# Performance work log

Hardware: AMD Instinct MI355X
Metric: run time of the kernel (lower is better)

The kernel has to match this reference:

```python
import jax, jax.numpy as jnp
import numpy as np

N_NODES = 100000
N_EDGES = 1600000
N_FEAT = 165
HIDDEN = 128
N_CLASSES = 2
NEG_SLOPE = 0.2


def setup_inputs() -> dict:
    key = jax.random.key(0)
    ks = jax.random.split(key, 16)
    s = 0.05
    return {
        'x': jax.random.normal(ks[0], (N_NODES, N_FEAT), jnp.float32),
        'edge_src': jax.random.randint(ks[1], (N_EDGES,), 0, N_NODES, jnp.int32),
        'edge_dst': jax.random.randint(ks[2], (N_EDGES,), 0, N_NODES, jnp.int32),
        'W1l': jax.random.normal(ks[3], (N_FEAT, HIDDEN), jnp.float32) * s,
        'b1l': jnp.zeros((HIDDEN,), jnp.float32),
        'W1r': jax.random.normal(ks[4], (N_FEAT, HIDDEN), jnp.float32) * s,
        'b1r': jnp.zeros((HIDDEN,), jnp.float32),
        'att1': jax.random.normal(ks[5], (HIDDEN,), jnp.float32) * s,
        'bias1': jnp.zeros((HIDDEN,), jnp.float32),
        'W2l': jax.random.normal(ks[6], (HIDDEN, N_CLASSES), jnp.float32) * s,
        'b2l': jnp.zeros((N_CLASSES,), jnp.float32),
        'W2r': jax.random.normal(ks[7], (HIDDEN, N_CLASSES), jnp.float32) * s,
        'b2r': jnp.zeros((N_CLASSES,), jnp.float32),
        'att2': jax.random.normal(ks[8], (N_CLASSES,), jnp.float32) * s,
        'bias2': jnp.zeros((N_CLASSES,), jnp.float32),
    }


def gatv2_conv(x, src, dst, Wl, bl, Wr, br, att, bias, n_nodes):
    # PyG GATv2Conv, heads=1: x_l for source/message, x_r for target
    xl = x @ Wl + bl            # [N, D_out]
    xr = x @ Wr + br            # [N, D_out]
    e = jax.nn.leaky_relu(xl[src] + xr[dst], NEG_SLOPE)  # [E, D_out]
    score = e @ att             # [E]
    # segment softmax over destination nodes (stable)
    m = jax.ops.segment_max(score, dst, num_segments=n_nodes)
    a = jnp.exp(score - m[dst])
    denom = jax.ops.segment_sum(a, dst, num_segments=n_nodes)
    alpha = a / denom[dst]      # [E]
    out = jax.ops.segment_sum(alpha[:, None] * xl[src], dst, num_segments=n_nodes)
    return out + bias


def reference(x, edge_src, edge_dst, W1l, b1l, W1r, b1r, att1, bias1,
              W2l, b2l, W2r, b2r, att2, bias2):
    n = x.shape[0]
    # GATv2Conv adds self loops by default; every node has >=1 incoming edge
    loops = jnp.arange(n, dtype=edge_src.dtype)
    src = jnp.concatenate([edge_src, loops])
    dst = jnp.concatenate([edge_dst, loops])
    h = gatv2_conv(x, src, dst, W1l, b1l, W1r, b1r, att1, bias1, n)
    h = jax.nn.relu(h)
    # F.dropout with training=False is identity (eval mode)
    out = gatv2_conv(h, src, dst, W2l, b2l, W2r, b2r, att2, bias2, n)
    return out
```

## Files before the change

### kernel.cpp

```cpp
#include <hip/hip_runtime.h>
#include <hip/hip_bf16.h>

#define N_NODES 100000
#define NPAD 100032
#define N_EDGES 1600000
#define ETOT (N_EDGES + N_NODES)
#define NFEAT 165
#define KP 192
#define HID 128
#define NCLS 2
#define NEG 0.2f

#define NBUCK 391
#define CHUNK 4096
#define NCHUNK 416
#define TOT4 ((NBUCK * NCHUNK) / 4)
#define NSB ((TOT4 + 511) / 512)
#define GS_BLOCKS 2048
#define REPACK_BLKS (NPAD / 64)

typedef short bf16x8 __attribute__((ext_vector_type(8)));
typedef float f32x4 __attribute__((ext_vector_type(4)));

#define OFF_FLAG 0
#define OFF_W 16
#define WO_ATT1 42496
#define WO_BIAS1 42624
#define WO_W2L 42752
#define WO_B2L 43008
#define WO_W2R 43010
#define WO_B2R 43266
#define WO_ATT2 43268
#define WO_BIAS2 43270

#define OFF_XB   43392
#define OFF_XP   OFF_XB
#define OFF_WT   (OFF_XB + NPAD * KP / 2)
#define OFF_BCAT (OFF_WT + 256 * KP / 2)
#define OFF_XLB  (OFF_BCAT + 256)
#define OFF_XRB  (OFF_XLB + NPAD * HID / 2)
#define OFF_PAIRS (OFF_XRB + NPAD * HID / 2)
#define OFF_CSR  (OFF_PAIRS + 2 * ETOT)
#define OFF_ROWPTR (OFF_CSR + ETOT)
#define OFF_S    (OFF_ROWPTR + N_NODES + 8)
#define OFF_XL2  (OFF_S + NBUCK * NCHUNK + 8)
#define OFF_XR2  (OFF_XL2 + N_NODES * NCLS)
#define OFF_H    (OFF_XR2 + N_NODES * NCLS)
#define OFF_DL   (OFF_H + N_NODES * HID)
#define OFF_DR   (OFF_DL + NPAD)
#define OFF_W2A  (OFF_DR + NPAD)
#define OFF_BSUM (OFF_W2A + 512)

__device__ __forceinline__ float bload16(unsigned short u) {
    return __uint_as_float(((unsigned)u) << 16);
}

__device__ __forceinline__ float lrelu(float v) {
    return fmaf(0.4f, fabsf(v), 0.6f * v);
}

__device__ __forceinline__ void unpack8(uint4 q, float* f) {
    f[0] = __uint_as_float(q.x << 16); f[1] = __uint_as_float(q.x & 0xffff0000u);
    f[2] = __uint_as_float(q.y << 16); f[3] = __uint_as_float(q.y & 0xffff0000u);
    f[4] = __uint_as_float(q.z << 16); f[5] = __uint_as_float(q.z & 0xffff0000u);
    f[6] = __uint_as_float(q.w << 16); f[7] = __uint_as_float(q.w & 0xffff0000u);
}

__device__ __forceinline__ unsigned short f2b(float f) {
    __hip_bfloat16 b = __float2bfloat16(f);
    return *(unsigned short*)&b;
}

__device__ __forceinline__ unsigned pack2(float a, float b) {
    return (unsigned)f2b(a) | ((unsigned)f2b(b) << 16);
}

__device__ __forceinline__ unsigned detect_flag(const unsigned short* x16, int lane) {
    unsigned short hh = x16[lane];
    unsigned e = (hh >> 7) & 0xFF;
    bool pl = ((hh & 0x7FFF) == 0) || (e >= 100 && e <= 140);
    unsigned long long m = __ballot(pl);
    return (__popcll(m) >= 52) ? 1u : 0u;
}

#define PREP_WT 49152
#define PREP_BC (PREP_WT + 256)
#define PREP_TOT (PREP_BC + 776)
#define PREP_BLKS ((PREP_TOT + 255) / 256)
__global__ void __launch_bounds__(256) k_prep_hist(
        const int* __restrict__ edst, int* __restrict__ bh,
        const unsigned short* __restrict__ x16,
        const void* W1l, const void* b1l, const void* W1r, const void* b1r,
        const void* att1, const void* bias1, const void* W2l, const void* b2l,
        const void* W2r, const void* b2r, const void* att2, const void* bias2,
        unsigned* __restrict__ flagp, unsigned short* __restrict__ wt,
        float* __restrict__ bcat, float* __restrict__ wb,
        float* __restrict__ w2a, unsigned short* __restrict__ xp) {
    __shared__ int hist[NBUCK];
    if (blockIdx.x < NCHUNK) {
        for (int i = threadIdx.x; i < NBUCK; i += 256) hist[i] = 0;
        __syncthreads();
        int base = blockIdx.x * CHUNK;
        for (int i = threadIdx.x; i < CHUNK; i += 256) {
            int e = base + i;
            if (e >= ETOT) break;
            int d = (e < N_EDGES) ? edst[e] : (e - N_EDGES);
            atomicAdd(&hist[d >> 8], 1);
        }
        __syncthreads();
        for (int b = threadIdx.x; b < NBUCK; b += 256)
            bh[b * NCHUNK + blockIdx.x] = hist[b];
        return;
    }
    int lane = threadIdx.x & 63;
    unsigned isbf = detect_flag(x16, lane);
    const float* xf = (const float*)x16;

    if (blockIdx.x >= NCHUNK + PREP_BLKS) {
        int node0 = (blockIdx.x - NCHUNK - PREP_BLKS) * 64;
        for (int i = threadIdx.x; i < 64 * (KP / 8); i += 256) {
            int r = i / (KP / 8);
            int c0 = (i - r * (KP / 8)) * 8;
            int grow = node0 + r;
            unsigned short hh[8];
#pragma unroll
            for (int j = 0; j < 8; j++) {
                int c = c0 + j;
                unsigned short v = 0;
                if (grow < N_NODES && c < NFEAT) {
                    size_t g = (size_t)grow * NFEAT + c;
                    v = isbf ? x16[g] : f2b(xf[g]);
                }
                hh[j] = v;
            }
            uint4 o;
            o.x = (unsigned)hh[0] | ((unsigned)hh[1] << 16);
            o.y = (unsigned)hh[2] | ((unsigned)hh[3] << 16);
            o.z = (unsigned)hh[4] | ((unsigned)hh[5] << 16);
            o.w = (unsigned)hh[6] | ((unsigned)hh[7] << 16);
            *(uint4*)&xp[(size_t)grow * KP + c0] = o;
        }
        return;
    }

    int i = (blockIdx.x - NCHUNK) * 256 + threadIdx.x;
    if (i == 0) *flagp = isbf;
    if (i >= PREP_TOT) return;
    if (i < PREP_WT) {
        int n = i / KP, k = i - n * KP;
        unsigned short v = 0;
        if (k < NFEAT) {
            const void* src = (n < HID) ? W1l : W1r;
            size_t off = (size_t)k * HID + (n & (HID - 1));
            v = isbf ? ((const unsigned short*)src)[off]
                     : f2b(((const float*)src)[off]);
        }
        wt[i] = v;
    } else if (i < PREP_BC) {
        int n = i - PREP_WT;
        const void* src = (n < HID) ? b1l : b1r;
        int off = n & (HID - 1);
        bcat[n] = isbf ? bload16(((const unsigned short*)src)[off])
                       : ((const float*)src)[off];
    } else {
        int j = i - PREP_BC;
        const void* src; int off; int dst;
        if      (j < 128) { src = att1;  off = j;       dst = WO_ATT1 + j; }
        else if (j < 256) { src = bias1; off = j - 128; dst = WO_BIAS1 + (j - 128); }
        else if (j < 512) { src = W2l;   off = j - 256; dst = WO_W2L + (j - 256); }
        else if (j < 514) { src = b2l;   off = j - 512; dst = WO_B2L + (j - 512); }
        else if (j < 770) { src = W2r;   off = j - 514; dst = WO_W2R + (j - 514); }
        else if (j < 772) { src = b2r;   off = j - 770; dst = WO_B2R + (j - 770); }
        else if (j < 774) { src = att2;  off = j - 772; dst = WO_ATT2 + (j - 772); }
        else              { src = bias2; off = j - 774; dst = WO_BIAS2 + (j - 774); }
        float val = isbf ? bload16(((const unsigned short*)src)[off])
                         : ((const float*)src)[off];
        wb[dst] = val;
        if (j >= 256 && j < 512) w2a[j - 256] = val;
        else if (j >= 514 && j < 770) w2a[256 + (j - 514)] = val;
    }
}

__global__ void __launch_bounds__(512) k_scan1(const int* __restrict__ S,
                                               int* __restrict__ bsum) {
    __shared__ int lds[512];
    int t = threadIdx.x;
    int i = blockIdx.x * 512 + t;
    const uint4* S4 = (const uint4*)S;
    int v = 0;
    if (i < TOT4) {
        uint4 q = S4[i];
        v = (int)(q.x + q.y + q.z + q.w);
    }
    lds[t] = v;
    __syncthreads();
    for (int off = 256; off > 0; off >>= 1) {
        if (t < off) lds[t] += lds[t + off];
        __syncthreads();
    }
    if (t == 0) bsum[blockIdx.x] = lds[0];
}

__global__ void __launch_bounds__(128) k_scan2(int* __restrict__ bsum) {
    __shared__ int lds[128];
    int t = threadIdx.x;
    int v = (t < NSB) ? bsum[t] : 0;
    lds[t] = v;
    __syncthreads();
    for (int off = 1; off < 128; off <<= 1) {
        int x = lds[t];
        if (t >= off) x += lds[t - off];
        __syncthreads();
        lds[t] = x;
        __syncthreads();
    }
    if (t < NSB) bsum[t] = (t == 0) ? 0 : lds[t - 1];
}

__global__ void __launch_bounds__(512) k_scan3(int* __restrict__ S,
                                               const int* __restrict__ bsum,
                                               int* __restrict__ rowptr) {
    __shared__ int lds[512];
    int t = threadIdx.x, b = blockIdx.x;
    int i = b * 512 + t;
    uint4* S4 = (uint4*)S;
    uint4 q = {0, 0, 0, 0};
    if (i < TOT4) q = S4[i];
    int s = (int)(q.x + q.y + q.z + q.w);
    lds[t] = s;
    __syncthreads();
    for (int off = 1; off < 512; off <<= 1) {
        int x = lds[t];
        if (t >= off) x += lds[t - off];
        __syncthreads();
        lds[t] = x;
        __syncthreads();
    }
    int excl = ((t == 0) ? 0 : lds[t - 1]) + bsum[b];
    if (i < TOT4) {
        uint4 o;
        o.x = excl;
        o.y = excl + q.x;
        o.z = excl + q.x + q.y;
        o.w = excl + q.x + q.y + q.z;
        S4[i] = o;
    }
    if (b == 0 && t == 0) rowptr[N_NODES] = ETOT;
}

__global__ void __launch_bounds__(256) k_scatter(const int* __restrict__ esrc,
                                                 const int* __restrict__ edst,
                                                 const int* __restrict__ S,
                                                 unsigned* __restrict__ pairs) {
    __shared__ int cur[NBUCK];
    for (int i = threadIdx.x; i < NBUCK; i += 256)
        cur[i] = S[i * NCHUNK + blockIdx.x];
    __syncthreads();
    int base = blockIdx.x * CHUNK;
    for (int i = threadIdx.x; i < CHUNK; i += 256) {
        int e = base + i;
        if (e >= ETOT) break;
        int s = (e < N_EDGES) ? esrc[e] : (e - N_EDGES);
        int d = (e < N_EDGES) ? edst[e] : (e - N_EDGES);
        int p = atomicAdd(&cur[d >> 8], 1);
        pairs[p] = (unsigned)s | ((unsigned)(d & 255) << 24);
    }
}

__global__ void __launch_bounds__(256) k_gemm1(
        const unsigned short* __restrict__ xp,
        const unsigned short* __restrict__ wt, const float* __restrict__ bcat,
        const float* __restrict__ attp,
        __hip_bfloat16* __restrict__ xlb, __hip_bfloat16* __restrict__ xrb,
        float* __restrict__ dl, float* __restrict__ dr) {
    __shared__ float dpart[4][64];
    int tid = threadIdx.x;
    int wave = tid >> 6, lane = tid & 63;
    int quad = lane >> 4, li = lane & 15;
    int node0 = blockIdx.x * 64;

    bf16x8 wfrag[4][6];
#pragma unroll
    for (int q = 0; q < 4; q++) {
        int n = wave * 64 + q * 16 + li;
#pragma unroll
        for (int kk = 0; kk < 6; kk++)
            wfrag[q][kk] = *(const bf16x8*)&wt[(size_t)n * KP + kk * 32 + quad * 8];
    }
    float4 bv[4], attq4[4];
    int colbase = (wave & 1) * 64;
#pragma unroll
    for (int q = 0; q < 4; q++) {
        bv[q] = *(const float4*)&bcat[wave * 64 + q * 16 + quad * 4];
        attq4[q] = *(const float4*)&attp[colbase + q * 16 + quad * 4];
    }

    for (int mt = 0; mt < 4; mt++) {
        int node = node0 + mt * 16 + li;
        bf16x8 xfrag[6];
#pragma unroll
        for (int kk = 0; kk < 6; kk++)
            xfrag[kk] = *(const bf16x8*)&xp[(size_t)node * KP + kk * 32 + quad * 8];
        __hip_bfloat16* dst = (wave < 2) ? xlb : xrb;
        float dp = 0.f;
#pragma unroll
        for (int q = 0; q < 4; q++) {
            f32x4 a = {0.f, 0.f, 0.f, 0.f};
#pragma unroll
            for (int kk = 0; kk < 6; kk++)
                a = __builtin_amdgcn_mfma_f32_16x16x32_bf16(wfrag[q][kk], xfrag[kk], a, 0, 0, 0);
            float f0 = a[0] + bv[q].x, f1 = a[1] + bv[q].y;
            float f2 = a[2] + bv[q].z, f3 = a[3] + bv[q].w;
            dp = fmaf(f0, attq4[q].x, dp);
            dp = fmaf(f1, attq4[q].y, dp);
            dp = fmaf(f2, attq4[q].z, dp);
            dp = fmaf(f3, attq4[q].w, dp);
            uint2 val = { pack2(f0, f1), pack2(f2, f3) };
            int col = colbase + q * 16 + quad * 4;
            *(uint2*)&dst[(size_t)node * HID + col] = val;
        }
        dp += __shfl_xor(dp, 16);
        dp += __shfl_xor(dp, 32);
        if (lane < 16) dpart[wave][mt * 16 + li] = dp;
    }
    __syncthreads();
    if (tid < 64)
        dl[node0 + tid] = dpart[0][tid] + dpart[1][tid];
    else if (tid < 128)
        dr[node0 + tid - 64] = dpart[2][tid - 64] + dpart[3][tid - 64];
}

__global__ void __launch_bounds__(256) k_bsort(const int* __restrict__ S,
                                               const unsigned* __restrict__ pairs,
                                               int* __restrict__ rowptr,
                                               int* __restrict__ csr) {
    __shared__ int hist[256];
    __shared__ int cur[256];
    int b = blockIdx.x, t = threadIdx.x;
    int beg = S[b * NCHUNK];
    int end = (b == NBUCK - 1) ? ETOT : S[(b + 1) * NCHUNK];
    hist[t] = 0;
    __syncthreads();
    for (int j = beg + t; j < end; j += 256)
        atomicAdd(&hist[pairs[j] >> 24], 1);
    __syncthreads();
    for (int off = 1; off < 256; off <<= 1) {
        int v = hist[t];
        if (t >= off) v += hist[t - off];
        __syncthreads();
        hist[t] = v;
        __syncthreads();
    }
    int excl = (t == 0) ? 0 : hist[t - 1];
    int node = b * 256 + t;
    if (node < N_NODES) rowptr[node] = beg + excl;
    cur[t] = beg + excl;
    __syncthreads();
    for (int j = beg + t; j < end; j += 256) {
        unsigned pr = pairs[j];
        int p = atomicAdd(&cur[pr >> 24], 1);
        csr[p] = (int)(pr & 0xFFFFFFu);
    }
}

__global__ void __launch_bounds__(256) k_gat1(const int* __restrict__ rowptr,
                                              const int* __restrict__ csr,
                                              const __hip_bfloat16* __restrict__ xlb,
                                              const __hip_bfloat16* __restrict__ xrb,
                                              const float* __restrict__ att,
                                              const float* __restrict__ bias,
                                              const float* __restrict__ dotsl,
                                              const float* __restrict__ dotsr,
                                              unsigned short* __restrict__ h16) {
    int wave = threadIdx.x >> 6, lane = threadIdx.x & 63;
    int sub = lane >> 4, li = lane & 15;
    float atv[8];
    {
        float4 t0 = ((const float4*)att)[li * 2];
        float4 t1 = ((const float4*)att)[li * 2 + 1];
        atv[0] = 0.4f * t0.x; atv[1] = 0.4f * t0.y;
        atv[2] = 0.4f * t0.z; atv[3] = 0.4f * t0.w;
        atv[4] = 0.4f * t1.x; atv[5] = 0.4f * t1.y;
        atv[6] = 0.4f * t1.z; atv[7] = 0.4f * t1.w;
    }

    for (int d = blockIdx.x * 4 + wave; d < N_NODES; d += GS_BLOCKS * 4) {
        uint4 qr = ((const uint4*)(xrb + (size_t)d * HID))[li];
        float xrv[8]; unpack8(qr, xrv);
        float drd = dotsr[d];
        int beg = rowptr[d], end = rowptr[d + 1];
        int iters = (end - beg + 3) >> 2;
        float l = 0.f, o[8];
#pragma unroll
        for (int t = 0; t < 8; t++) o[t] = 0.f;

        int j = beg + sub;
        bool valid = j < end;
        int s = valid ? csr[j] : 0;
        uint4 q = *(const uint4*)(xlb + (size_t)s * HID + li * 8);
        float dlc = dotsl[s];

        for (int it = 0; it < iters; it++) {
            float c[8]; unpack8(q, c);
            bool v = valid;
            float dle = dlc;
            j += 4;
            valid = j < end;
            int sn = valid ? csr[j] : 0;
            q = *(const uint4*)(xlb + (size_t)sn * HID + li * 8);
            dlc = dotsl[sn];

            float pa = 0.f;
#pragma unroll
            for (int t = 0; t < 8; t++) {
                float vv = c[t] + xrv[t];
                pa = fmaf(atv[t], fabsf(vv), pa);
            }
            pa += __shfl_xor(pa, 1);
            pa += __shfl_xor(pa, 2);
            pa += __shfl_xor(pa, 4);
            pa += __shfl_xor(pa, 8);
            float p = fmaf(0.6f, dle + drd, pa);
            float a = v ? __expf(p) : 0.f;
            l += a;
#pragma unroll
            for (int t = 0; t < 8; t++) o[t] = fmaf(a, c[t], o[t]);
        }
        l += __shfl_xor(l, 16);
        l += __shfl_xor(l, 32);
#pragma unroll
        for (int t = 0; t < 8; t++) {
            o[t] += __shfl_xor(o[t], 16);
            o[t] += __shfl_xor(o[t], 32);
        }
        if (sub == 0) {
            float inv = 1.f / l;
            float4 bv0 = ((const float4*)bias)[li * 2];
            float4 bv1 = ((const float4*)bias)[li * 2 + 1];
            float r0 = fmaxf(fmaf(o[0], inv, bv0.x), 0.f);
            float r1 = fmaxf(fmaf(o[1], inv, bv0.y), 0.f);
            float r2 = fmaxf(fmaf(o[2], inv, bv0.z), 0.f);
            float r3 = fmaxf(fmaf(o[3], inv, bv0.w), 0.f);
            float r4 = fmaxf(fmaf(o[4], inv, bv1.x), 0.f);
            float r5 = fmaxf(fmaf(o[5], inv, bv1.y), 0.f);
            float r6 = fmaxf(fmaf(o[6], inv, bv1.z), 0.f);
            float r7 = fmaxf(fmaf(o[7], inv, bv1.w), 0.f);
            uint4 val = { pack2(r0, r1), pack2(r2, r3),
                          pack2(r4, r5), pack2(r6, r7) };
            *(uint4*)&h16[(size_t)d * HID + li * 8] = val;
        }
    }
}

__global__ void __launch_bounds__(256) k_gemm2(const unsigned short* __restrict__ h16,
                                               const float* __restrict__ wb,
                                               const float* __restrict__ w2a,
                                               float* __restrict__ xl2, float* __restrict__ xr2) {
    int wave = threadIdx.x >> 6, lane = threadIdx.x & 63;
    int node = blockIdx.x * 4 + wave;
    if (node >= N_NODES) return;
    unsigned hw = ((const unsigned*)(h16 + (size_t)node * HID))[lane];
    float h0 = __uint_as_float(hw << 16);
    float h1 = __uint_as_float(hw & 0xffff0000u);
    float4 wl = ((const float4*)w2a)[lane];
    float4 wr = ((const float4*)(w2a + 256))[lane];
    float al0 = h0 * wl.x + h1 * wl.z;
    float al1 = h0 * wl.y + h1 * wl.w;
    float ar0 = h0 * wr.x + h1 * wr.z;
    float ar1 = h0 * wr.y + h1 * wr.w;
#pragma unroll
    for (int off = 32; off > 0; off >>= 1) {
        al0 += __shfl_down(al0, off);
        al1 += __shfl_down(al1, off);
        ar0 += __shfl_down(ar0, off);
        ar1 += __shfl_down(ar1, off);
    }
    if (lane == 0) {
        xl2[node * 2 + 0] = al0 + wb[WO_B2L + 0];
        xl2[node * 2 + 1] = al1 + wb[WO_B2L + 1];
        xr2[node * 2 + 0] = ar0 + wb[WO_B2R + 0];
        xr2[node * 2 + 1] = ar1 + wb[WO_B2R + 1];
    }
}

__global__ void __launch_bounds__(256) k_gat2(const int* __restrict__ rowptr,
                                              const int* __restrict__ csr,
                                              const float* __restrict__ xl2,
                                              const float* __restrict__ xr2,
                                              const float* __restrict__ wb,
                                              const unsigned* __restrict__ flag,
                                              void* __restrict__ dout) {
    int t = blockIdx.x * 256 + threadIdx.x;
    int d = t >> 2, part = t & 3;
    if (d >= N_NODES) return;
    float xr0 = xr2[d * 2 + 0], xr1 = xr2[d * 2 + 1];
    float at0 = wb[WO_ATT2], at1 = wb[WO_ATT2 + 1];
    int beg = rowptr[d], end = rowptr[d + 1];
    float l = 0.f, o0 = 0.f, o1 = 0.f;
    for (int j = beg + part; j < end; j += 4) {
        int s = csr[j];
        float b0 = xl2[s * 2 + 0], b1 = xl2[s * 2 + 1];
        float p = at0 * lrelu(b0 + xr0) + at1 * lrelu(b1 + xr1);
        float a = __expf(p);
        l += a;
        o0 = fmaf(a, b0, o0);
        o1 = fmaf(a, b1, o1);
    }
    l += __shfl_xor(l, 1);  o0 += __shfl_xor(o0, 1);  o1 += __shfl_xor(o1, 1);
    l += __shfl_xor(l, 2);  o0 += __shfl_xor(o0, 2);  o1 += __shfl_xor(o1, 2);
    if (part == 0) {
        float inv = 1.f / l;
        float v0 = fmaf(o0, inv, wb[WO_BIAS2 + 0]);
        float v1 = fmaf(o1, inv, wb[WO_BIAS2 + 1]);
        if (*flag) {
            ((__hip_bfloat16*)dout)[d * 2 + 0] = __float2bfloat16(v0);
            ((__hip_bfloat16*)dout)[d * 2 + 1] = __float2bfloat16(v1);
        } else {
            ((float*)dout)[d * 2 + 0] = v0;
            ((float*)dout)[d * 2 + 1] = v1;
        }
    }
}

extern "C" void kernel_launch(void* const* d_in, const int* in_sizes, int n_in,
                              void* d_out, int out_size, void* d_ws, size_t ws_size,
                              hipStream_t stream) {
    char* w = (char*)d_ws;
    unsigned* flag = (unsigned*)(w + (size_t)OFF_FLAG * 4);
    float* wb = (float*)(w + (size_t)OFF_W * 4);
    unsigned short* xp = (unsigned short*)(w + (size_t)OFF_XP * 4);
    unsigned short* wt = (unsigned short*)(w + (size_t)OFF_WT * 4);
    float* bcat = (float*)(w + (size_t)OFF_BCAT * 4);
    __hip_bfloat16* xlb = (__hip_bfloat16*)(w + (size_t)OFF_XLB * 4);
    __hip_bfloat16* xrb = (__hip_bfloat16*)(w + (size_t)OFF_XRB * 4);
    unsigned* pairs = (unsigned*)(w + (size_t)OFF_PAIRS * 4);
    int* csr = (int*)(w + (size_t)OFF_CSR * 4);
    int* rowptr = (int*)(w + (size_t)OFF_ROWPTR * 4);
    int* S = (int*)(w + (size_t)OFF_S * 4);
    float* xl2 = (float*)(w + (size_t)OFF_XL2 * 4);
    float* xr2 = (float*)(w + (size_t)OFF_XR2 * 4);
    unsigned short* h16 = (unsigned short*)(w + (size_t)OFF_H * 4);
    float* dl = (float*)(w + (size_t)OFF_DL * 4);
    float* dr = (float*)(w + (size_t)OFF_DR * 4);
    float* w2a = (float*)(w + (size_t)OFF_W2A * 4);
    int* bsum = (int*)(w + (size_t)OFF_BSUM * 4);
    const int* esrc = (const int*)d_in[1];
    const int* edst = (const int*)d_in[2];

    k_prep_hist<<<NCHUNK + PREP_BLKS + REPACK_BLKS, 256, 0, stream>>>(
        edst, S, (const unsigned short*)d_in[0],
        d_in[3], d_in[4], d_in[5], d_in[6], d_in[7], d_in[8],
        d_in[9], d_in[10], d_in[11], d_in[12], d_in[13], d_in[14],
        flag, wt, bcat, wb, w2a, xp);

    k_scan1<<<NSB, 512, 0, stream>>>(S, bsum);
    k_scan2<<<1, 128, 0, stream>>>(bsum);
    k_scan3<<<NSB, 512, 0, stream>>>(S, bsum, rowptr);

    k_scatter<<<NCHUNK, 256, 0, stream>>>(esrc, edst, S, pairs);

    k_bsort<<<NBUCK, 256, 0, stream>>>(S, pairs, rowptr, csr);

    k_gemm1<<<NPAD / 64, 256, 0, stream>>>(xp, wt, bcat,
                                           wb + WO_ATT1, xlb, xrb, dl, dr);

    k_gat1<<<GS_BLOCKS, 256, 0, stream>>>(rowptr, csr, xlb, xrb,
                                          wb + WO_ATT1, wb + WO_BIAS1,
                                          dl, dr, h16);

    k_gemm2<<<(N_NODES + 3) / 4, 256, 0, stream>>>(h16, wb, w2a, xl2, xr2);

    k_gat2<<<(4 * N_NODES + 255) / 256, 256, 0, stream>>>(rowptr, csr, xl2, xr2,
                                                          wb, flag, d_out);
}
```

Measured before the change: 368.9 us.

## Overlap layer-1 GEMM with edge scatter and bucket sort launches

Splits the layer-1 GEMM tiles across the scatter and bucket-sort kernels as extra blocks, so independent GEMM work runs alongside the graph CSR construction. This removes one kernel launch and fills idle compute units during the memory-bound sort phases. Shared memory is reused through a union. The split ratio is fixed at 782 of the 1563 tiles for the scatter launch, and GEMM blocks may compete with the sort blocks for bandwidth.

Result: faster. 361.6 us (-2.0%).

```diff
diff --git a/kernel.cpp b/kernel.cpp
--- a/kernel.cpp
+++ b/kernel.cpp
@@ -18,6 +18,9 @@
 #define NSB ((TOT4 + 511) / 512)
 #define GS_BLOCKS 2048
 #define REPACK_BLKS (NPAD / 64)
+#define G1TOT (NPAD / 64)
+#define G1A 782
+#define G1B (G1TOT - G1A)
 
 typedef short bf16x8 __attribute__((ext_vector_type(8)));
 typedef float f32x4 __attribute__((ext_vector_type(4)));
@@ -248,36 +251,15 @@
     if (b == 0 && t == 0) rowptr[N_NODES] = ETOT;
 }
 
-__global__ void __launch_bounds__(256) k_scatter(const int* __restrict__ esrc,
-                                                 const int* __restrict__ edst,
-                                                 const int* __restrict__ S,
-                                                 unsigned* __restrict__ pairs) {
-    __shared__ int cur[NBUCK];
-    for (int i = threadIdx.x; i < NBUCK; i += 256)
-        cur[i] = S[i * NCHUNK + blockIdx.x];
-    __syncthreads();
-    int base = blockIdx.x * CHUNK;
-    for (int i = threadIdx.x; i < CHUNK; i += 256) {
-        int e = base + i;
-        if (e >= ETOT) break;
-        int s = (e < N_EDGES) ? esrc[e] : (e - N_EDGES);
-        int d = (e < N_EDGES) ? edst[e] : (e - N_EDGES);
-        int p = atomicAdd(&cur[d >> 8], 1);
-        pairs[p] = (unsigned)s | ((unsigned)(d & 255) << 24);
-    }
-}
-
-__global__ void __launch_bounds__(256) k_gemm1(
+__device__ __forceinline__ void gemm1_tile(
+        int node0, int tid, float (*dpart)[64],
         const unsigned short* __restrict__ xp,
         const unsigned short* __restrict__ wt, const float* __restrict__ bcat,
         const float* __restrict__ attp,
         __hip_bfloat16* __restrict__ xlb, __hip_bfloat16* __restrict__ xrb,
         float* __restrict__ dl, float* __restrict__ dr) {
-    __shared__ float dpart[4][64];
-    int tid = threadIdx.x;
     int wave = tid >> 6, lane = tid & 63;
     int quad = lane >> 4, li = lane & 15;
-    int node0 = blockIdx.x * 64;
 
     bf16x8 wfrag[4][6];
 #pragma unroll
@@ -330,37 +312,75 @@
         dr[node0 + tid - 64] = dpart[2][tid - 64] + dpart[3][tid - 64];
 }
 
-__global__ void __launch_bounds__(256) k_bsort(const int* __restrict__ S,
-                                               const unsigned* __restrict__ pairs,
-                                               int* __restrict__ rowptr,
-                                               int* __restrict__ csr) {
-    __shared__ int hist[256];
-    __shared__ int cur[256];
+__global__ void __launch_bounds__(256) k_scatter_gemm1(
+        const int* __restrict__ esrc, const int* __restrict__ edst,
+        const int* __restrict__ S, unsigned* __restrict__ pairs,
+        const unsigned short* __restrict__ xp,
+        const unsigned short* __restrict__ wt, const float* __restrict__ bcat,
+        const float* __restrict__ attp,
+        __hip_bfloat16* __restrict__ xlb, __hip_bfloat16* __restrict__ xrb,
+        float* __restrict__ dl, float* __restrict__ dr) {
+    __shared__ union { int cur[NBUCK]; float dpart[4][64]; } u;
+    if (blockIdx.x < NCHUNK) {
+        for (int i = threadIdx.x; i < NBUCK; i += 256)
+            u.cur[i] = S[i * NCHUNK + blockIdx.x];
+        __syncthreads();
+        int base = blockIdx.x * CHUNK;
+        for (int i = threadIdx.x; i < CHUNK; i += 256) {
+            int e = base + i;
+            if (e >= ETOT) break;
+            int s = (e < N_EDGES) ? esrc[e] : (e - N_EDGES);
+            int d = (e < N_EDGES) ? edst[e] : (e - N_EDGES);
+            int p = atomicAdd(&u.cur[d >> 8], 1);
+            pairs[p] = (unsigned)s | ((unsigned)(d & 255) << 24);
+        }
+        return;
+    }
+    int node0 = (blockIdx.x - NCHUNK) * 64;
+    gemm1_tile(node0, threadIdx.x, u.dpart, xp, wt, bcat, attp,
+               xlb, xrb, dl, dr);
+}
+
+__global__ void __launch_bounds__(256) k_bsort_gemm1(
+        const int* __restrict__ S, const unsigned* __restrict__ pairs,
+        int* __restrict__ rowptr, int* __restrict__ csr,
+        const unsigned short* __restrict__ xp,
+        const unsigned short* __restrict__ wt, const float* __restrict__ bcat,
+        const float* __restrict__ attp,
+        __hip_bfloat16* __restrict__ xlb, __hip_bfloat16* __restrict__ xrb,
+        float* __restrict__ dl, float* __restrict__ dr) {
+    __shared__ union { struct { int hist[256]; int cur[256]; } s;
+                       float dpart[4][64]; } u;
     int b = blockIdx.x, t = threadIdx.x;
-    int beg = S[b * NCHUNK];
-    int end = (b == NBUCK - 1) ? ETOT : S[(b + 1) * NCHUNK];
-    hist[t] = 0;
-    __syncthreads();
-    for (int j = beg + t; j < end; j += 256)
-        atomicAdd(&hist[pairs[j] >> 24], 1);
-    __syncthreads();
-    for (int off = 1; off < 256; off <<= 1) {
-        int v = hist[t];
-        if (t >= off) v += hist[t - off];
-        __syncthreads();
-        hist[t] = v;
-        __syncthreads();
-    }
-    int excl = (t == 0) ? 0 : hist[t - 1];
-    int node = b * 256 + t;
-    if (node < N_NODES) rowptr[node] = beg + excl;
-    cur[t] = beg + excl;
-    __syncthreads();
-    for (int j = beg + t; j < end; j += 256) {
-        unsigned pr = pairs[j];
-        int p = atomicAdd(&cur[pr >> 24], 1);
-        csr[p] = (int)(pr & 0xFFFFFFu);
-    }
+    if (b < NBUCK) {
+        int beg = S[b * NCHUNK];
+        int end = (b == NBUCK - 1) ? ETOT : S[(b + 1) * NCHUNK];
+        u.s.hist[t] = 0;
+        __syncthreads();
+        for (int j = beg + t; j < end; j += 256)
+            atomicAdd(&u.s.hist[pairs[j] >> 24], 1);
+        __syncthreads();
+        for (int off = 1; off < 256; off <<= 1) {
+            int v = u.s.hist[t];
+            if (t >= off) v += u.s.hist[t - off];
+            __syncthreads();
+            u.s.hist[t] = v;
+            __syncthreads();
+        }
+        int excl = (t == 0) ? 0 : u.s.hist[t - 1];
+        int node = b * 256 + t;
+        if (node < N_NODES) rowptr[node] = beg + excl;
+        u.s.cur[t] = beg + excl;
+        __syncthreads();
+        for (int j = beg + t; j < end; j += 256) {
+            unsigned pr = pairs[j];
+            int p = atomicAdd(&u.s.cur[pr >> 24], 1);
+            csr[p] = (int)(pr & 0xFFFFFFu);
+        }
+        return;
+    }
+    int node0 = (G1A + (b - NBUCK)) * 64;
+    gemm1_tile(node0, t, u.dpart, xp, wt, bcat, attp, xlb, xrb, dl, dr);
 }
 
 __global__ void __launch_bounds__(256) k_gat1(const int* __restrict__ rowptr,
@@ -557,12 +577,13 @@
     k_scan2<<<1, 128, 0, stream>>>(bsum);
     k_scan3<<<NSB, 512, 0, stream>>>(S, bsum, rowptr);
 
-    k_scatter<<<NCHUNK, 256, 0, stream>>>(esrc, edst, S, pairs);
-
-    k_bsort<<<NBUCK, 256, 0, stream>>>(S, pairs, rowptr, csr);
-
-    k_gemm1<<<NPAD / 64, 256, 0, stream>>>(xp, wt, bcat,
-                                           wb + WO_ATT1, xlb, xrb, dl, dr);
+    k_scatter_gemm1<<<NCHUNK + G1A, 256, 0, stream>>>(
+        esrc, edst, S, pairs, xp, wt, bcat,
+        wb + WO_ATT1, xlb, xrb, dl, dr);
+
+    k_bsort_gemm1<<<NBUCK + G1B, 256, 0, stream>>>(
+        S, pairs, rowptr, csr, xp, wt, bcat,
+        wb + WO_ATT1, xlb, xrb, dl, dr);
 
     k_gat1<<<GS_BLOCKS, 256, 0, stream>>>(rowptr, csr, xlb, xrb,
                                           wb + WO_ATT1, wb + WO_BIAS1,
```

## Fuse x repack into gemm1 via LDS staging and merge with histogram kernel

Applied to the files above, without the earlier changes.

Removes the separate pass that converted x into a padded bf16 buffer in global memory. The first-layer GEMM now loads x directly, converts it and stages it in LDS with a padded stride, and runs in the same launch as the edge histogram blocks. A small prep kernel that writes the weights and flag is split out and runs first. The goal is to avoid writing and re-reading the padded x buffer and to overlap the GEMM with the histogram pass. The cost is an extra launch and an element-wise, uncoalesced load of x into LDS.

After: 411.7 us. 11.6% more time.

```diff
diff --git a/kernel.cpp b/kernel.cpp
--- a/kernel.cpp
+++ b/kernel.cpp
@@ -17,7 +17,6 @@
 #define TOT4 ((NBUCK * NCHUNK) / 4)
 #define NSB ((TOT4 + 511) / 512)
 #define GS_BLOCKS 2048
-#define REPACK_BLKS (NPAD / 64)
 
 typedef short bf16x8 __attribute__((ext_vector_type(8)));
 typedef float f32x4 __attribute__((ext_vector_type(4)));
@@ -34,7 +33,6 @@
 #define WO_BIAS2 43270
 
 #define OFF_XB   43392
-#define OFF_XP   OFF_XB
 #define OFF_WT   (OFF_XB + NPAD * KP / 2)
 #define OFF_BCAT (OFF_WT + 256 * KP / 2)
 #define OFF_XLB  (OFF_BCAT + 256)
@@ -87,63 +85,17 @@
 #define PREP_BC (PREP_WT + 256)
 #define PREP_TOT (PREP_BC + 776)
 #define PREP_BLKS ((PREP_TOT + 255) / 256)
-__global__ void __launch_bounds__(256) k_prep_hist(
-        const int* __restrict__ edst, int* __restrict__ bh,
+__global__ void __launch_bounds__(256) k_prep0(
         const unsigned short* __restrict__ x16,
         const void* W1l, const void* b1l, const void* W1r, const void* b1r,
         const void* att1, const void* bias1, const void* W2l, const void* b2l,
         const void* W2r, const void* b2r, const void* att2, const void* bias2,
         unsigned* __restrict__ flagp, unsigned short* __restrict__ wt,
         float* __restrict__ bcat, float* __restrict__ wb,
-        float* __restrict__ w2a, unsigned short* __restrict__ xp) {
-    __shared__ int hist[NBUCK];
-    if (blockIdx.x < NCHUNK) {
-        for (int i = threadIdx.x; i < NBUCK; i += 256) hist[i] = 0;
-        __syncthreads();
-        int base = blockIdx.x * CHUNK;
-        for (int i = threadIdx.x; i < CHUNK; i += 256) {
-            int e = base + i;
-            if (e >= ETOT) break;
-            int d = (e < N_EDGES) ? edst[e] : (e - N_EDGES);
-            atomicAdd(&hist[d >> 8], 1);
-        }
-        __syncthreads();
-        for (int b = threadIdx.x; b < NBUCK; b += 256)
-            bh[b * NCHUNK + blockIdx.x] = hist[b];
-        return;
-    }
+        float* __restrict__ w2a) {
     int lane = threadIdx.x & 63;
     unsigned isbf = detect_flag(x16, lane);
-    const float* xf = (const float*)x16;
-
-    if (blockIdx.x >= NCHUNK + PREP_BLKS) {
-        int node0 = (blockIdx.x - NCHUNK - PREP_BLKS) * 64;
-        for (int i = threadIdx.x; i < 64 * (KP / 8); i += 256) {
-            int r = i / (KP / 8);
-            int c0 = (i - r * (KP / 8)) * 8;
-            int grow = node0 + r;
-            unsigned short hh[8];
-#pragma unroll
-            for (int j = 0; j < 8; j++) {
-                int c = c0 + j;
-                unsigned short v = 0;
-                if (grow < N_NODES && c < NFEAT) {
-                    size_t g = (size_t)grow * NFEAT + c;
-                    v = isbf ? x16[g] : f2b(xf[g]);
-                }
-                hh[j] = v;
-            }
-            uint4 o;
-            o.x = (unsigned)hh[0] | ((unsigned)hh[1] << 16);
-            o.y = (unsigned)hh[2] | ((unsigned)hh[3] << 16);
-            o.z = (unsigned)hh[4] | ((unsigned)hh[5] << 16);
-            o.w = (unsigned)hh[6] | ((unsigned)hh[7] << 16);
-            *(uint4*)&xp[(size_t)grow * KP + c0] = o;
-        }
-        return;
-    }
-
-    int i = (blockIdx.x - NCHUNK) * 256 + threadIdx.x;
+    int i = blockIdx.x * 256 + threadIdx.x;
     if (i == 0) *flagp = isbf;
     if (i >= PREP_TOT) return;
     if (i < PREP_WT) {
@@ -181,6 +133,106 @@
     }
 }
 
+#define XS_STRIDE 200
+__global__ void __launch_bounds__(256) k_hist_gemm1(
+        const int* __restrict__ edst, int* __restrict__ bh,
+        const void* __restrict__ x, const unsigned* __restrict__ flagp,
+        const unsigned short* __restrict__ wt, const float* __restrict__ bcat,
+        const float* __restrict__ attp,
+        __hip_bfloat16* __restrict__ xlb, __hip_bfloat16* __restrict__ xrb,
+        float* __restrict__ dl, float* __restrict__ dr) {
+    __shared__ union {
+        int hist[NBUCK];
+        struct { unsigned short xs[64 * XS_STRIDE]; float dpart[4][64]; } g;
+    } u;
+
+    if (blockIdx.x < NCHUNK) {
+        for (int i = threadIdx.x; i < NBUCK; i += 256) u.hist[i] = 0;
+        __syncthreads();
+        int base = blockIdx.x * CHUNK;
+        for (int i = threadIdx.x; i < CHUNK; i += 256) {
+            int e = base + i;
+            if (e >= ETOT) break;
+            int d = (e < N_EDGES) ? edst[e] : (e - N_EDGES);
+            atomicAdd(&u.hist[d >> 8], 1);
+        }
+        __syncthreads();
+        for (int b = threadIdx.x; b < NBUCK; b += 256)
+            bh[b * NCHUNK + blockIdx.x] = u.hist[b];
+        return;
+    }
+
+    int tid = threadIdx.x;
+    int wave = tid >> 6, lane = tid & 63;
+    int quad = lane >> 4, li = lane & 15;
+    int node0 = (blockIdx.x - NCHUNK) * 64;
+    unsigned isbf = *flagp;
+    const float* xf = (const float*)x;
+    const unsigned short* x16 = (const unsigned short*)x;
+
+    for (int i = tid; i < 64 * XS_STRIDE; i += 256) {
+        int r = i / XS_STRIDE, c = i - r * XS_STRIDE;
+        int grow = node0 + r;
+        unsigned short v = 0;
+        if (c < NFEAT && grow < N_NODES) {
+            size_t g = (size_t)grow * NFEAT + c;
+            v = isbf ? x16[g] : f2b(xf[g]);
+        }
+        u.g.xs[i] = v;
+    }
+
+    bf16x8 wfrag[4][6];
+#pragma unroll
+    for (int q = 0; q < 4; q++) {
+        int n = wave * 64 + q * 16 + li;
+#pragma unroll
+        for (int kk = 0; kk < 6; kk++)
+            wfrag[q][kk] = *(const bf16x8*)&wt[(size_t)n * KP + kk * 32 + quad * 8];
+    }
+    float4 bv[4], attq4[4];
+    int colbase = (wave & 1) * 64;
+#pragma unroll
+    for (int q = 0; q < 4; q++) {
+        bv[q] = *(const float4*)&bcat[wave * 64 + q * 16 + quad * 4];
+        attq4[q] = *(const float4*)&attp[colbase + q * 16 + quad * 4];
+    }
+    __syncthreads();
+
+    for (int mt = 0; mt < 4; mt++) {
+        bf16x8 xfrag[6];
+#pragma unroll
+        for (int kk = 0; kk < 6; kk++)
+            xfrag[kk] = *(const bf16x8*)&u.g.xs[(mt * 16 + li) * XS_STRIDE + kk * 32 + quad * 8];
+        int node = node0 + mt * 16 + li;
+        __hip_bfloat16* dst = (wave < 2) ? xlb : xrb;
+        float dp = 0.f;
+#pragma unroll
+        for (int q = 0; q < 4; q++) {
+            f32x4 a = {0.f, 0.f, 0.f, 0.f};
+#pragma unroll
+            for (int kk = 0; kk < 6; kk++)
+                a = __builtin_amdgcn_mfma_f32_16x16x32_bf16(wfrag[q][kk], xfrag[kk], a, 0, 0, 0);
+            float f0 = a[0] + bv[q].x, f1 = a[1] + bv[q].y;
+            float f2 = a[2] + bv[q].z, f3 = a[3] + bv[q].w;
+            dp = fmaf(f0, attq4[q].x, dp);
+            dp = fmaf(f1, attq4[q].y, dp);
+            dp = fmaf(f2, attq4[q].z, dp);
+            dp = fmaf(f3, attq4[q].w, dp);
+            uint2 val = { pack2(f0, f1), pack2(f2, f3) };
+            int col = colbase + q * 16 + quad * 4;
+            *(uint2*)&dst[(size_t)node * HID + col] = val;
+        }
+        dp += __shfl_xor(dp, 16);
+        dp += __shfl_xor(dp, 32);
+        if (lane < 16) u.g.dpart[wave][mt * 16 + li] = dp;
+    }
+    __syncthreads();
+    if (tid < 64)
+        dl[node0 + tid] = u.g.dpart[0][tid] + u.g.dpart[1][tid];
+    else if (tid < 128)
+        dr[node0 + tid - 64] = u.g.dpart[2][tid - 64] + u.g.dpart[3][tid - 64];
+}
+
 __global__ void __launch_bounds__(512) k_scan1(const int* __restrict__ S,
                                                int* __restrict__ bsum) {
     __shared__ int lds[512];
@@ -265,69 +317,6 @@
         int p = atomicAdd(&cur[d >> 8], 1);
         pairs[p] = (unsigned)s | ((unsigned)(d & 255) << 24);
     }
-}
-
-__global__ void __launch_bounds__(256) k_gemm1(
-        const unsigned short* __restrict__ xp,
-        const unsigned short* __restrict__ wt, const float* __restrict__ bcat,
-        const float* __restrict__ attp,
-        __hip_bfloat16* __restrict__ xlb, __hip_bfloat16* __restrict__ xrb,
-        float* __restrict__ dl, float* __restrict__ dr) {
-    __shared__ float dpart[4][64];
-    int tid = threadIdx.x;
-    int wave = tid >> 6, lane = tid & 63;
-    int quad = lane >> 4, li = lane & 15;
-    int node0 = blockIdx.x * 64;
-
-    bf16x8 wfrag[4][6];
-#pragma unroll
-    for (int q = 0; q < 4; q++) {
-        int n = wave * 64 + q * 16 + li;
-#pragma unroll
-        for (int kk = 0; kk < 6; kk++)
-            wfrag[q][kk] = *(const bf16x8*)&wt[(size_t)n * KP + kk * 32 + quad * 8];
-    }
-    float4 bv[4], attq4[4];
-    int colbase = (wave & 1) * 64;
-#pragma unroll
-    for (int q = 0; q < 4; q++) {
-        bv[q] = *(const float4*)&bcat[wave * 64 + q * 16 + quad * 4];
-        attq4[q] = *(const float4*)&attp[colbase + q * 16 + quad * 4];
-    }
-
-    for (int mt = 0; mt < 4; mt++) {
-        int node = node0 + mt * 16 + li;
-        bf16x8 xfrag[6];
-#pragma unroll
-        for (int kk = 0; kk < 6; kk++)
-            xfrag[kk] = *(const bf16x8*)&xp[(size_t)node * KP + kk * 32 + quad * 8];
-        __hip_bfloat16* dst = (wave < 2) ? xlb : xrb;
-        float dp = 0.f;
-#pragma unroll
-        for (int q = 0; q < 4; q++) {
-            f32x4 a = {0.f, 0.f, 0.f, 0.f};
-#pragma unroll
-            for (int kk = 0; kk < 6; kk++)
-                a = __builtin_amdgcn_mfma_f32_16x16x32_bf16(wfrag[q][kk], xfrag[kk], a, 0, 0, 0);
-            float f0 = a[0] + bv[q].x, f1 = a[1] + bv[q].y;
-            float f2 = a[2] + bv[q].z, f3 = a[3] + bv[q].w;
-            dp = fmaf(f0, attq4[q].x, dp);
-            dp = fmaf(f1, attq4[q].y, dp);
-            dp = fmaf(f2, attq4[q].z, dp);
-            dp = fmaf(f3, attq4[q].w, dp);
-            uint2 val = { pack2(f0, f1), pack2(f2, f3) };
-            int col = colbase + q * 16 + quad * 4;
-            *(uint2*)&dst[(size_t)node * HID + col] = val;
-        }
-        dp += __shfl_xor(dp, 16);
-        dp += __shfl_xor(dp, 32);
-        if (lane < 16) dpart[wave][mt * 16 + li] = dp;
-    }
-    __syncthreads();
-    if (tid < 64)
-        dl[node0 + tid] = dpart[0][tid] + dpart[1][tid];
-    else if (tid < 128)
-        dr[node0 + tid - 64] = dpart[2][tid - 64] + dpart[3][tid - 64];
 }
 
 __global__ void __launch_bounds__(256) k_bsort(const int* __restrict__ S,
@@ -528,7 +517,6 @@
     char* w = (char*)d_ws;
     unsigned* flag = (unsigned*)(w + (size_t)OFF_FLAG * 4);
     float* wb = (float*)(w + (size_t)OFF_W * 4);
-    unsigned short* xp = (unsigned short*)(w + (size_t)OFF_XP * 4);
     unsigned short* wt = (unsigned short*)(w + (size_t)OFF_WT * 4);
     float* bcat = (float*)(w + (size_t)OFF_BCAT * 4);
     __hip_bfloat16* xlb = (__hip_bfloat16*)(w + (size_t)OFF_XLB * 4);
@@ -547,11 +535,15 @@
     const int* esrc = (const int*)d_in[1];
     const int* edst = (const int*)d_in[2];
 
-    k_prep_hist<<<NCHUNK + PREP_BLKS + REPACK_BLKS, 256, 0, stream>>>(
-        edst, S, (const unsigned short*)d_in[0],
+    k_prep0<<<PREP_BLKS, 256, 0, stream>>>(
+        (const unsigned short*)d_in[0],
         d_in[3], d_in[4], d_in[5], d_in[6], d_in[7], d_in[8],
         d_in[9], d_in[10], d_in[11], d_in[12], d_in[13], d_in[14],
-        flag, wt, bcat, wb, w2a, xp);
+        flag, wt, bcat, wb, w2a);
+
+    k_hist_gemm1<<<NCHUNK + NPAD / 64, 256, 0, stream>>>(
+        edst, S, d_in[0], flag, wt, bcat,
+        wb + WO_ATT1, xlb, xrb, dl, dr);
 
     k_scan1<<<NSB, 512, 0, stream>>>(S, bsum);
     k_scan2<<<1, 128, 0, stream>>>(bsum);
@@ -561,9 +553,6 @@
 
     k_bsort<<<NBUCK, 256, 0, stream>>>(S, pairs, rowptr, csr);
 
-    k_gemm1<<<NPAD / 64, 256, 0, stream>>>(xp, wt, bcat,
-                                           wb + WO_ATT1, xlb, xrb, dl, dr);
-
     k_gat1<<<GS_BLOCKS, 256, 0, stream>>>(rowptr, csr, xlb, xrb,
                                           wb + WO_ATT1, wb + WO_BIAS1,
                                           dl, dr, h16);
```
